# Performance work log

Hardware: AMD Instinct MI355X
Metric: run time of the kernel (lower is better)

Reference implementation:

```python
import jax, jax.numpy as jnp
import numpy as np

B, G, S, GS, P = 32, 512, 128, 32, 10
C, H, RED = 384, 6, 16
HID = 4 * C
D = C // H
SCALE = D ** -0.5

def _gelu(x):
    return jax.nn.gelu(x, approximate=False)

def _ln(x, g, b):
    m = jnp.mean(x, -1, keepdims=True)
    v = jnp.var(x, -1, keepdims=True)
    return (x - m) * jax.lax.rsqrt(v + 1e-5) * g + b

def _split_qkv(x, W):
    Bn, T, Cc = x.shape
    qkv = (x @ W).reshape(Bn, T, 3, H, D).transpose(2, 0, 3, 1, 4)
    return qkv[0], qkv[1], qkv[2]

def _merge(x):
    Bn, Hh, T, Dd = x.shape
    return x.transpose(0, 2, 1, 3).reshape(Bn, T, Hh * Dd)

def _mha(q, k, v):
    a = jax.nn.softmax(jnp.einsum('bhnd,bhmd->bhnm', q, k) * SCALE, axis=-1)
    return jnp.einsum('bhnm,bhmd->bhnd', a, v)

def _forward(x, center1, center2, neighborhood, prompt_embeddings, ln1_g, ln1_b, Wqkv, Wproj, bproj, gate, ln2_g, ln2_b, W1, b1, W2, b2, ad_down_W, ad_down_b, ad_up_W, ad_up_b, ad_gate, bn_g, bn_b, bn_mean, bn_var, ln3_g, ln3_b, a1_Wqkv, a1_Wproj, a1_bproj, ad1_down_W, ad1_down_b, ad1_up_W, ad1_up_b, idx, center_idx, group_size, if_maxmean, pro_cof, center_cof):
    Bx, Ntok, Cc = x.shape
    # prompt dropout is identity in eval
    prompt = jnp.broadcast_to(prompt_embeddings, (Bx, P, Cc))
    # --- gated dual self / prompt-cross attention ---
    xn = _ln(x, ln1_g, ln1_b)
    q, k, v = _split_qkv(xn, Wqkv)
    xs = _mha(q, k, v)                                  # [B,H,N,D]
    _, pk, pv = _split_qkv(prompt, Wqkv)
    pa = jax.nn.softmax(jnp.einsum('bhnd,bhpd->bhnp', q, pk) * SCALE, axis=-1)
    px = jnp.einsum('bhnp,bhpd->bhnd', gate * pa, pv)   # learned gate per head
    x = x + (_merge(xs) + _merge(px)) @ Wproj + bproj
    # --- MLP + gated bottleneck adapter residual ---
    h = _gelu(_ln(x, ln2_g, ln2_b) @ W1 + b1) @ W2 + b2
    h_ad = h + _gelu(h @ ad_down_W + ad_down_b) @ ad_up_W + ad_up_b
    x = ad_gate * h_ad + x
    cls_x = x[:, :1]
    xt = x[:, 1:]                                       # [B,G,C]
    flat = xt.reshape(Bx * G, Cc)
    x_nb = flat[idx].reshape(Bx * S, group_size, Cc)    # KNN neighborhoods
    x_ct = flat[center_idx].reshape(Bx, S, Cc)          # center features
    # NOTE: original normalizes `neighborhood` by its std, but result is unused
    # --- local self-attention (attn1 over norm3) on each neighborhood ---
    nq, nk, nv = _split_qkv(_ln(x_nb, ln3_g, ln3_b), a1_Wqkv)
    no = _mha(nq, nk, nv)
    x_nb = x_nb + _merge(no) @ a1_Wproj + a1_bproj
    knn = x_nb.reshape(Bx, S, group_size, Cc)
    lc = jnp.max(knn, axis=2)
    if if_maxmean:
        lc = lc + jnp.mean(knn, axis=2)
    # BatchNorm1d (eval, running stats) + GELU over channel dim
    lc = _gelu((lc - bn_mean) * jax.lax.rsqrt(bn_var + 1e-5) * bn_g + bn_b)
    vis = lc + center_cof * x_ct                        # [B,S,C]
    # --- propagate: de_neighbors == S so sorted-topk == full weighted sum ---
    d = jnp.sum((center1[:, :, None, :] - center2[:, None, :, :]) ** 2, axis=-1)  # [B,G,S]
    w = 1.0 / (d + 1e-8)
    w = w / jnp.sum(w, axis=-1, keepdims=True)
    interp = jnp.einsum('bns,bsc->bnc', w, vis)
    xt = xt + pro_cof * interp
    out = jnp.concatenate([cls_x, xt], axis=1)
    # adapter1
    out = out + _gelu(out @ ad1_down_W + ad1_down_b) @ ad1_up_W + ad1_up_b
    return out

def setup_inputs():
    ks = jax.random.split(jax.random.key(0), 20)
    r = lambda i, shape, s=0.02: jax.random.normal(ks[i], shape, jnp.float32) * s
    return {
        'x': jax.random.normal(ks[0], (B, G + 1, C), jnp.float32),
        'center1': jax.random.normal(ks[1], (B, G, 3), jnp.float32),
        'center2': jax.random.normal(ks[2], (B, S, 3), jnp.float32),
        'neighborhood': jax.random.normal(ks[3], (B, S, GS, 3), jnp.float32),
        'prompt_embeddings': r(4, (P, C)),
        'ln1_g': jnp.ones(C), 'ln1_b': jnp.zeros(C),
        'Wqkv': r(5, (C, 3 * C)),
        'Wproj': r(6, (C, C)), 'bproj': jnp.zeros(C),
        'gate': jax.random.normal(ks[7], (1, H, 1, 1), jnp.float32),
        'ln2_g': jnp.ones(C), 'ln2_b': jnp.zeros(C),
        'W1': r(8, (C, HID)), 'b1': jnp.zeros(HID),
        'W2': r(9, (HID, C)), 'b2': jnp.zeros(C),
        'ad_down_W': r(10, (C, RED)), 'ad_down_b': jnp.zeros(RED),
        'ad_up_W': r(11, (RED, C)), 'ad_up_b': jnp.zeros(C),
        'ad_gate': jax.random.normal(ks[12], (), jnp.float32),
        'bn_g': jnp.ones(C), 'bn_b': jnp.zeros(C),
        'bn_mean': jnp.zeros(C), 'bn_var': jnp.ones(C),
        'ln3_g': jnp.ones(C), 'ln3_b': jnp.zeros(C),
        'a1_Wqkv': r(13, (C, 3 * C)),
        'a1_Wproj': r(14, (C, C)), 'a1_bproj': jnp.zeros(C),
        'ad1_down_W': r(15, (C, RED)), 'ad1_down_b': jnp.zeros(RED),
        'ad1_up_W': r(16, (RED, C)), 'ad1_up_b': jnp.zeros(C),
        'idx': jax.random.randint(ks[17], (B * S * GS,), 0, B * G),
        'center_idx': jax.random.randint(ks[18], (B * S,), 0, B * G),
        'group_size': GS,
        'if_maxmean': 1,
        'pro_cof': 1,
        'center_cof': 1,
    }

def reference(x, center1, center2, neighborhood, prompt_embeddings, ln1_g, ln1_b, Wqkv, Wproj, bproj, gate, ln2_g, ln2_b, W1, b1, W2, b2, ad_down_W, ad_down_b, ad_up_W, ad_up_b, ad_gate, bn_g, bn_b, bn_mean, bn_var, ln3_g, ln3_b, a1_Wqkv, a1_Wproj, a1_bproj, ad1_down_W, ad1_down_b, ad1_up_W, ad1_up_b, idx, center_idx, group_size, if_maxmean, pro_cof, center_cof):
    return _forward(x, center1, center2, neighborhood, prompt_embeddings, ln1_g, ln1_b, Wqkv, Wproj, bproj, gate, ln2_g, ln2_b, W1, b1, W2, b2, ad_down_W, ad_down_b, ad_up_W, ad_up_b, ad_gate, bn_g, bn_b, bn_mean, bn_var, ln3_g, ln3_b, a1_Wqkv, a1_Wproj, a1_bproj, ad1_down_W, ad1_down_b, ad1_up_W, ad1_up_b, idx, center_idx, group_size, if_maxmean, pro_cof, center_cof)
```

## Files before the change

kernel.cpp:

```cpp
#include <hip/hip_runtime.h>
#include <hip/hip_bf16.h>
#include <cstdint>
#include <cstddef>

typedef __hip_bfloat16 bf16;
constexpr int TOK = 32 * 513;

typedef __attribute__((ext_vector_type(8))) short short8;
typedef __attribute__((ext_vector_type(4))) float f32x4;

__device__ __forceinline__ float bflo(unsigned u){ return __uint_as_float(u << 16); }
__device__ __forceinline__ float bfhi(unsigned u){ return __uint_as_float(u & 0xffff0000u); }
__device__ __forceinline__ float b2f(bf16 x){ return __bfloat162float(x); }
__device__ __forceinline__ bf16  f2b(float x){ return __float2bfloat16(x); }
__device__ __forceinline__ float geluf(float x){ return 0.5f*x*(1.0f + erff(x*0.70710678118654752f)); }
__device__ __forceinline__ float scal(const int* p){
  const int i = *p;
  if (i > -1000000 && i < 1000000) return (float)i;
  return __int_as_float(i);
}
__device__ __forceinline__ f32x4 mfma16(short8 a, short8 b, f32x4 c){
  return __builtin_amdgcn_mfma_f32_16x16x32_bf16(a, b, c, 0, 0, 0);
}
__device__ __forceinline__ int swzl(int l){ return l ^ ((l >> 3) & 7); }
__device__ __forceinline__ void gload_lds16(const bf16* g, bf16* l){
  __builtin_amdgcn_global_load_lds(
      (const __attribute__((address_space(1))) void*)g,
      (__attribute__((address_space(3))) void*)l, 16, 0, 0);
}

__global__ __launch_bounds__(256) void detect_kernel(const unsigned* __restrict__ x,
                                                     int* __restrict__ flag)
{
  const int t = threadIdx.x;
  bool bad = false;
  for (int i = t; i < 2048; i += 256){
    const unsigned u = x[i];
    const float a = fabsf(bflo(u)), b = fabsf(bfhi(u));
    if (!(a < 1e6f) || !(b < 1e6f)) bad = true;
  }
  __shared__ int s;
  if (t == 0) s = 0;
  __syncthreads();
  const unsigned long long m = __ballot(bad);
  if (m != 0ull && (t & 63) == 0) atomicOr(&s, 1);
  __syncthreads();
  if (t == 0) *flag = s;
}

struct ConvArgs {
  const void* src[34];
  bf16*       dst[34];
  int         n[34];
};
__global__ __launch_bounds__(256) void convert_many(const int* __restrict__ flag, ConvArgs a)
{
  const int ii = blockIdx.y;
  const bool isf = (*flag != 0);
  const int n = a.n[ii];
  const int n8 = n >> 3;
  bf16* d = a.dst[ii];
  if (isf){
    const float4* s = (const float4*)a.src[ii];
    for (int i = blockIdx.x*256 + threadIdx.x; i < n8; i += gridDim.x*256){
      const float4 f0 = s[i*2];
      const float4 f1 = s[i*2 + 1];
      bf16 tmp[8] = {f2b(f0.x),f2b(f0.y),f2b(f0.z),f2b(f0.w),
                     f2b(f1.x),f2b(f1.y),f2b(f1.z),f2b(f1.w)};
      *(uint4*)(d + (size_t)i*8) = *(const uint4*)tmp;
    }
  } else {
    const uint4* s = (const uint4*)a.src[ii];
    for (int i = blockIdx.x*256 + threadIdx.x; i < n8; i += gridDim.x*256){
      ((uint4*)d)[i] = s[i];
    }
  }
  if (blockIdx.x == 0){
    for (int i = n8*8 + threadIdx.x; i < n; i += 256){
      d[i] = isf ? f2b(((const float*)a.src[ii])[i]) : ((const bf16*)a.src[ii])[i];
    }
  }
}

struct ShufArgs {
  const bf16* W[6];
  bf16*       out[6];
  int         N[6];
  int         KT[6];
  int         NT[6];
};
__global__ __launch_bounds__(256) void shuffle_many(ShufArgs a)
{
  const int ii = blockIdx.y;
  const int id = blockIdx.x*256 + threadIdx.x;
  const int KT = a.KT[ii], NT = a.NT[ii], N = a.N[ii];
  if (id >= NT*KT*64) return;
  const int l  = id & 63;
  const int k0 = (id >> 6) % KT;
  const int n0 = (id >> 6) / KT;
  const bf16* W = a.W[ii];
  bf16 tmp[8];
  #pragma unroll
  for (int j = 0; j < 8; j++)
    tmp[j] = W[(size_t)(k0*32 + (l>>4)*8 + j)*N + n0*16 + (l&15)];
  *(uint4*)(a.out[ii] + (size_t)id*8) = *(const uint4*)tmp;
}

template<bool SRC_BF16>
__global__ __launch_bounds__(256) void ln_kernel(const void* __restrict__ src,
    const bf16* __restrict__ g, const bf16* __restrict__ b,
    bf16* __restrict__ out, int rows)
{
  const int wave = (blockIdx.x * blockDim.x + threadIdx.x) >> 6;
  const int lane = threadIdx.x & 63;
  if (wave >= rows) return;
  float v[6]; float s = 0.f, s2 = 0.f;
  #pragma unroll
  for (int i = 0; i < 6; i++){
    const int c = lane + 64*i;
    float x;
    if (SRC_BF16) x = b2f(((const bf16*)src)[(size_t)wave*384 + c]);
    else          x = ((const float*)src)[(size_t)wave*384 + c];
    v[i] = x; s += x; s2 += x*x;
  }
  #pragma unroll
  for (int mm = 32; mm; mm >>= 1){ s += __shfl_xor(s, mm); s2 += __shfl_xor(s2, mm); }
  const float mean = s * (1.f/384.f);
  const float rs = rsqrtf(s2 * (1.f/384.f) - mean*mean + 1e-5f);
  #pragma unroll
  for (int i = 0; i < 6; i++){
    const int c = lane + 64*i;
    out[(size_t)wave*384 + c] = f2b((v[i]-mean)*rs*b2f(g[c]) + b2f(b[c]));
  }
}

template<int EPI>
__global__ __launch_bounds__(256) void mfma_gemm(
    const bf16* __restrict__ A, const bf16* __restrict__ Bsh,
    const bf16* __restrict__ bias, const bf16* __restrict__ resid,
    void* __restrict__ outv, int M, int N, int K)
{
  __shared__ __align__(16) bf16 sA[8*64*8];
  const int t = threadIdx.x, lane = t & 63, w = t >> 6;
  const int l15 = lane & 15, quad = lane >> 4;
  const int wm = w & 1, wn = w >> 1;
  const int m0 = blockIdx.y * 128;
  const int n0t = blockIdx.x * 8 + wn * 4;
  const int KT = K >> 5;
  f32x4 acc[4][4];
  #pragma unroll
  for (int i = 0; i < 4; i++){
    #pragma unroll
    for (int j = 0; j < 4; j++) acc[i][j] = f32x4{0.f,0.f,0.f,0.f};
  }
  const int mtA = 2*w, mtB = 2*w + 1;
  const bf16* gA = A + (size_t)(m0 + mtA*16 + l15)*K + quad*8;
  const bf16* gB = A + (size_t)(m0 + mtB*16 + l15)*K + quad*8;
  bf16* lA = sA + mtA*512;
  bf16* lB = sA + mtB*512;

  for (int ks = 0; ks < KT; ks++){
    gload_lds16(gA + ks*32, lA);
    gload_lds16(gB + ks*32, lB);
    __syncthreads();
    short8 afr[4];
    #pragma unroll
    for (int i = 0; i < 4; i++)
      afr[i] = *(const short8*)(sA + (((wm*4+i)*64 + lane) << 3));
    #pragma unroll
    for (int j = 0; j < 4; j++){
      const short8 b = *(const short8*)(Bsh + ((size_t)((n0t+j)*KT + ks)*64 + lane)*8);
      #pragma unroll
      for (int i = 0; i < 4; i++) acc[i][j] = mfma16(afr[i], b, acc[i][j]);
    }
    __syncthreads();
  }
  #pragma unroll
  for (int i = 0; i < 4; i++){
    #pragma unroll
    for (int r = 0; r < 4; r++){
      const int gm = m0 + (wm*4+i)*16 + quad*4 + r;
      if (gm < M){
        #pragma unroll
        for (int j = 0; j < 4; j++){
          const int gn = (n0t+j)*16 + l15;
          float v = acc[i][j][r];
          const size_t o = (size_t)gm*N + gn;
          if (EPI == 0){ v += b2f(bias[gn]); ((bf16*)outv)[o] = f2b(v); }
          else if (EPI == 1){ ((bf16*)outv)[o] = f2b(v); }
          else if (EPI == 2){ v += b2f(bias[gn]); ((bf16*)outv)[o] = f2b(geluf(v)); }
          else { v += b2f(bias[gn]) + b2f(resid[o]); ((float*)outv)[o] = v; }
        }
      }
    }
  }
}

__global__ __launch_bounds__(256) void pqkv_kernel(const bf16* __restrict__ pe,
    const bf16* __restrict__ Wqkv, float* __restrict__ pq)
{
  const int n  = blockIdx.x*64 + (threadIdx.x & 63);
  const int rg = threadIdx.x >> 6;
  for (int r = rg; r < 10; r += 4){
    float s0 = 0.f, s1 = 0.f;
    for (int c = 0; c < 384; c += 2){
      s0 = fmaf(b2f(pe[(size_t)r*384+c]),   b2f(Wqkv[(size_t)c*1152 + n]),     s0);
      s1 = fmaf(b2f(pe[(size_t)r*384+c+1]), b2f(Wqkv[(size_t)(c+1)*1152 + n]), s1);
    }
    pq[(size_t)r*1152 + n] = s0 + s1;
  }
}

__global__ __launch_bounds__(256) void attn_kernel(
    const bf16* __restrict__ qkv, const float* __restrict__ pq,
    const bf16* __restrict__ gate, bf16* __restrict__ ao)
{
  __shared__ __align__(16) bf16 s_kf[2][8*64*8];
  __shared__ __align__(16) bf16 s_vT[64*72];
  __shared__ __align__(16) bf16 s_p[4*16*64];
  __shared__ __align__(16) bf16 s_pk[16*72];
  __shared__ __align__(16) bf16 s_pvT[64*40];
  const int bh = blockIdx.y;
  const int b = bh / 6, h = bh % 6;
  const int q0 = blockIdx.x * 64;
  const int t = threadIdx.x, lane = t & 63, w = t >> 6;
  const int l15 = lane & 15, quad = lane >> 4;

  const int qtok = q0 + w*16 + l15;
  const int qtokc = qtok < 513 ? qtok : 512;
  const bf16* qp = qkv + (size_t)(b*513 + qtokc)*1152 + h*64 + quad*8;
  const short8 qf0 = *(const short8*)qp;
  const short8 qf1 = *(const short8*)(qp + 32);

  auto issueK = [&](int kb, int buf){
    const int key = kb + w*16 + l15;
    const int keyc = key < 513 ? key : 512;
    const bf16* src = qkv + (size_t)(b*513 + keyc)*1152 + 384 + h*64 + quad*8;
    gload_lds16(src,      &s_kf[buf][((w*2 + 0)*64)*8]);
    gload_lds16(src + 32, &s_kf[buf][((w*2 + 1)*64)*8]);
  };

  const int kp = t & 31, dg = t >> 5;

  {
    const int j = t >> 4, dc = (t & 15) * 4;
    float f[4] = {0.f,0.f,0.f,0.f};
    if (j < 10){
      const float* pk = pq + (size_t)j*1152 + 384 + h*64 + dc;
      f[0]=pk[0]; f[1]=pk[1]; f[2]=pk[2]; f[3]=pk[3];
    }
    bf16 tmp[4] = {f2b(f[0]),f2b(f[1]),f2b(f[2]),f2b(f[3])};
    *(uint2*)(s_pk + j*72 + dc) = *(const uint2*)tmp;
  }
  {
    const int d = t & 63, kg = t >> 6;
    #pragma unroll
    for (int kk = 0; kk < 8; kk++){
      const int key = kg*8 + kk;
      bf16 v = f2b(0.f);
      if (key < 10) v = f2b(pq[(size_t)key*1152 + 768 + h*64 + d]);
      s_pvT[d*40 + key] = v;
    }
  }

  uint4 pv0 = {0,0,0,0}, pv1 = {0,0,0,0};
  {
    const int key0 = 2*kp;
    if (key0 < 513)
      pv0 = *(const uint4*)(qkv + (size_t)(b*513 + key0)*1152 + 768 + h*64 + dg*8);
    if (key0 + 1 < 513)
      pv1 = *(const uint4*)(qkv + (size_t)(b*513 + key0 + 1)*1152 + 768 + h*64 + dg*8);
  }
  issueK(0, 0);
  int cur = 0;

  float m_i[4], l_i[4];
  f32x4 oacc[4];
  #pragma unroll
  for (int r = 0; r < 4; r++){ m_i[r] = -30000.f; l_i[r] = 0.f; }
  #pragma unroll
  for (int nt = 0; nt < 4; nt++) oacc[nt] = f32x4{0.f,0.f,0.f,0.f};
  bf16* myp = s_p + w*16*64;

  for (int kt = 0; kt < 9; kt++){
    const int kb = kt*64;
    __syncthreads();
    {
      const unsigned short* a0 = (const unsigned short*)&pv0;
      const unsigned short* a1 = (const unsigned short*)&pv1;
      unsigned* vt = (unsigned*)s_vT;
      #pragma unroll
      for (int j = 0; j < 8; j++)
        vt[(dg*8 + j)*36 + kp] = (unsigned)a0[j] | ((unsigned)a1[j] << 16);
    }
    __syncthreads();

    f32x4 sreg[4];
    #pragma unroll
    for (int nt = 0; nt < 4; nt++){
      const short8 kf0 = *(const short8*)(&s_kf[cur][((nt*2 + 0)*64 + lane)*8]);
      const short8 kf1 = *(const short8*)(&s_kf[cur][((nt*2 + 1)*64 + lane)*8]);
      f32x4 acc = mfma16(qf0, kf0, f32x4{0.f,0.f,0.f,0.f});
      acc = mfma16(qf1, kf1, acc);
      const bool kvalid = (kb + nt*16 + l15) < 513;
      #pragma unroll
      for (int r = 0; r < 4; r++)
        sreg[nt][r] = kvalid ? acc[r]*0.125f : -30000.f;
    }

    if (kt < 8){
      issueK(kb + 64, cur ^ 1);
      const int key0 = kb + 64 + 2*kp;
      pv0 = {0,0,0,0}; pv1 = {0,0,0,0};
      if (key0 < 513)
        pv0 = *(const uint4*)(qkv + (size_t)(b*513 + key0)*1152 + 768 + h*64 + dg*8);
      if (key0 + 1 < 513)
        pv1 = *(const uint4*)(qkv + (size_t)(b*513 + key0 + 1)*1152 + 768 + h*64 + dg*8);
    }

    float alpha[4];
    #pragma unroll
    for (int r = 0; r < 4; r++){
      float mx = fmaxf(fmaxf(sreg[0][r], sreg[1][r]), fmaxf(sreg[2][r], sreg[3][r]));
      #pragma unroll
      for (int mm = 8; mm; mm >>= 1) mx = fmaxf(mx, __shfl_xor(mx, mm));
      const float mn = fmaxf(m_i[r], mx);
      alpha[r] = __expf(m_i[r] - mn);
      m_i[r] = mn;
      float ps = 0.f;
      #pragma unroll
      for (int nt = 0; nt < 4; nt++){
        const float p = __expf(sreg[nt][r] - mn);
        sreg[nt][r] = p; ps += p;
      }
      #pragma unroll
      for (int mm = 8; mm; mm >>= 1) ps += __shfl_xor(ps, mm);
      l_i[r] = l_i[r]*alpha[r] + ps;
    }
    #pragma unroll
    for (int nt = 0; nt < 4; nt++){
      #pragma unroll
      for (int r = 0; r < 4; r++)
        myp[(quad*4 + r)*64 + nt*16 + l15] = f2b(sreg[nt][r]);
    }
    #pragma unroll
    for (int nt = 0; nt < 4; nt++){
      #pragma unroll
      for (int r = 0; r < 4; r++) oacc[nt][r] *= alpha[r];
    }
    const short8* ap = (const short8*)(myp + l15*64);
    #pragma unroll
    for (int nt = 0; nt < 4; nt++){
      const short8* bv = (const short8*)(s_vT + (nt*16 + l15)*72);
      oacc[nt] = mfma16(ap[quad],     bv[quad],     oacc[nt]);
      oacc[nt] = mfma16(ap[4 + quad], bv[4 + quad], oacc[nt]);
    }
    cur ^= 1;
  }

  f32x4 sp;
  {
    f32x4 acc = f32x4{0.f,0.f,0.f,0.f};
    const short8* bp = (const short8*)(s_pk + l15*72);
    acc = mfma16(qf0, bp[quad],     acc);
    acc = mfma16(qf1, bp[4 + quad], acc);
    #pragma unroll
    for (int r = 0; r < 4; r++)
      sp[r] = (l15 < 10) ? acc[r]*0.125f : -30000.f;
  }
  float psr[4];
  #pragma unroll
  for (int r = 0; r < 4; r++){
    float mx = sp[r];
    #pragma unroll
    for (int mm = 8; mm; mm >>= 1) mx = fmaxf(mx, __shfl_xor(mx, mm));
    const float p = __expf(sp[r] - mx);
    float ps = p;
    #pragma unroll
    for (int mm = 8; mm; mm >>= 1) ps += __shfl_xor(ps, mm);
    psr[r] = ps;
    myp[(quad*4 + r)*64 + l15]      = f2b(p);
    myp[(quad*4 + r)*64 + 16 + l15] = f2b(0.f);
  }
  f32x4 pva[4];
  {
    const short8* ap = (const short8*)(myp + l15*64);
    #pragma unroll
    for (int nt = 0; nt < 4; nt++){
      const short8* bv = (const short8*)(s_pvT + (nt*16 + l15)*40);
      pva[nt] = mfma16(ap[quad], bv[quad], f32x4{0.f,0.f,0.f,0.f});
    }
  }

  const float gh = b2f(gate[h]);
  #pragma unroll
  for (int r = 0; r < 4; r++){
    const int tok = q0 + w*16 + quad*4 + r;
    if (tok < 513){
      const float invl = 1.f/l_i[r];
      const float gps  = gh/psr[r];
      #pragma unroll
      for (int nt = 0; nt < 4; nt++){
        const float val = oacc[nt][r]*invl + pva[nt][r]*gps;
        ao[(size_t)(b*513 + tok)*384 + h*64 + nt*16 + l15] = f2b(val);
      }
    }
  }
}

template<bool MID>
__global__ __launch_bounds__(256) void adapter_kernel(
    const void* __restrict__ src,
    const bf16* __restrict__ Wd, const bf16* __restrict__ bd,
    const bf16* __restrict__ Wu, const bf16* __restrict__ bu,
    const bf16* __restrict__ p_gate,
    const bf16* __restrict__ g3, const bf16* __restrict__ b3,
    const int* __restrict__ flag,
    float* __restrict__ xres, bf16* __restrict__ xln3,
    void* __restrict__ out)
{
  __shared__ float s_h[4][384];
  const int wv = threadIdx.x >> 6, lane = threadIdx.x & 63;
  const int row = blockIdx.x*4 + wv;
  float v[6];
  #pragma unroll
  for (int i = 0; i < 6; i++){
    const int c = lane + 64*i;
    float x;
    if (MID) x = b2f(((const bf16*)src)[(size_t)row*384 + c]);
    else     x = ((const float*)src)[(size_t)row*384 + c];
    v[i] = x; s_h[wv][c] = x;
  }
  const int o = lane & 15, p = lane >> 4;
  float part = 0.f;
  #pragma unroll 4
  for (int j = 0; j < 96; j++)
    part = fmaf(s_h[wv][p*96 + j], b2f(Wd[(size_t)(p*96 + j)*16 + o]), part);
  part += __shfl_xor(part, 16);
  part += __shfl_xor(part, 32);
  const float y = geluf(part + b2f(bd[o]));
  float up[6] = {0.f,0.f,0.f,0.f,0.f,0.f};
  #pragma unroll
  for (int o2 = 0; o2 < 16; o2++){
    const float yo = __shfl(y, o2);
    #pragma unroll
    for (int i = 0; i < 6; i++)
      up[i] = fmaf(yo, b2f(Wu[(size_t)o2*384 + lane + 64*i]), up[i]);
  }
  if (MID){
    const float g = b2f(p_gate[0]);
    float nv[6]; float s = 0.f, s2 = 0.f;
    #pragma unroll
    for (int i = 0; i < 6; i++){
      const int c = lane + 64*i;
      const float had = v[i] + up[i] + b2f(bu[c]);
      const float nx = g*had + xres[(size_t)row*384 + c];
      xres[(size_t)row*384 + c] = nx;
      nv[i] = nx; s += nx; s2 += nx*nx;
    }
    const int boff = row % 513;
    if (boff != 0){
      #pragma unroll
      for (int mm = 32; mm; mm >>= 1){ s += __shfl_xor(s, mm); s2 += __shfl_xor(s2, mm); }
      const float mean = s * (1.f/384.f);
      const float rs = rsqrtf(s2 * (1.f/384.f) - mean*mean + 1e-5f);
      const int r3 = (row/513)*512 + boff - 1;
      #pragma unroll
      for (int i = 0; i < 6; i++){
        const int c = lane + 64*i;
        xln3[(size_t)r3*384 + c] = f2b((nv[i]-mean)*rs*b2f(g3[c]) + b2f(b3[c]));
      }
    }
  } else {
    const bool isf = (*flag != 0);
    #pragma unroll
    for (int i = 0; i < 6; i++){
      const int c = lane + 64*i;
      const float ov = v[i] + up[i] + b2f(bu[c]);
      if (isf) ((float*)out)[(size_t)row*384 + c] = ov;
      else     ((bf16*)out)[(size_t)row*384 + c] = f2b(ov);
    }
  }
}

__global__ __launch_bounds__(512, 2) void local_kernel(
    const bf16* __restrict__ qkv3, const float* __restrict__ xres,
    const int* __restrict__ idx, const int* __restrict__ cidx,
    const bf16* __restrict__ Bp, const bf16* __restrict__ bp1,
    const bf16* __restrict__ bng, const bf16* __restrict__ bnb,
    const bf16* __restrict__ bnm, const bf16* __restrict__ bnv,
    const int* __restrict__ p_ifmm, const int* __restrict__ p_ccof,
    float* __restrict__ vis)
{
  __shared__ __align__(16) bf16 sV[3*4*64*8];
  __shared__ __align__(16) bf16 sP[3*2*64*8];
  __shared__ __align__(16) bf16 sO[3*4*64*8];
  __shared__ int s_flat[32];
  __shared__ int s_tok[32];

  const int g = blockIdx.x;
  const int t = threadIdx.x, lane = t & 63, w = t >> 6;
  const int l15 = lane & 15, quad = lane >> 4;
  const int lanez = swzl(lane);

  if (t < 32){
    const int r = idx[g*32 + t];
    s_flat[t] = r;
    s_tok[t]  = (r >> 9)*513 + 1 + (r & 511);
  }
  __syncthreads();

  const int vrowA = t & 31,          vccA = t >> 5;
  const int vrowB = (512 + t) & 31,  vccB = (512 + t) >> 5;
  const int vhA = vccA >> 3, vd0A = (vccA & 7) * 8;
  const int vhB = vccB >> 3, vd0B = (vccB & 7) * 8;
  const bool hasB = (t < 256);

  uint4 svA, svB;
  {
    svA = *(const uint4*)(qkv3 + (size_t)s_flat[vrowA]*1152 + 768 + (0*3 + vhA)*64 + vd0A);
    if (hasB) svB = *(const uint4*)(qkv3 + (size_t)s_flat[vrowB]*1152 + 768 + (0*3 + vhB)*64 + vd0B);
  }

  f32x4 accp[3][2];
  #pragma unroll
  for (int a = 0; a < 3; a++){
    #pragma unroll
    for (int m = 0; m < 2; m++) accp[a][m] = f32x4{0.f,0.f,0.f,0.f};
  }

  #pragma unroll
  for (int hc = 0; hc < 2; hc++){
    {
      const bf16* sa = (const bf16*)&svA;
      #pragma unroll
      for (int j2 = 0; j2 < 8; j2++){
        const int d = vd0A + j2;
        const int L = (vrowA>>3)*16 + (d&15);
        sV[((vhA*4 + (d>>4))*64 + swzl(L))*8 + (vrowA&7)] = sa[j2];
      }
      if (hasB){
        const bf16* sb = (const bf16*)&svB;
        #pragma unroll
        for (int j2 = 0; j2 < 8; j2++){
          const int d = vd0B + j2;
          const int L = (vrowB>>3)*16 + (d&15);
          sV[((vhB*4 + (d>>4))*64 + swzl(L))*8 + (vrowB&7)] = sb[j2];
        }
      }
    }
    __syncthreads();

    if (w < 6){
      const int h = w >> 1, mt = w & 1;
      const size_t qrow = (size_t)s_flat[mt*16 + l15]*1152;
      const int dcol = (hc*3 + h)*64 + quad*8;
      const short8 q0 = *(const short8*)(qkv3 + qrow + dcol);
      const short8 q1 = *(const short8*)(qkv3 + qrow + dcol + 32);
      f32x4 sr[2];
      #pragma unroll
      for (int nt = 0; nt < 2; nt++){
        const size_t krow = (size_t)s_flat[nt*16 + l15]*1152 + 384;
        const short8 k0 = *(const short8*)(qkv3 + krow + dcol);
        const short8 k1 = *(const short8*)(qkv3 + krow + dcol + 32);
        f32x4 acc = mfma16(q0, k0, f32x4{0.f,0.f,0.f,0.f});
        acc = mfma16(q1, k1, acc);
        #pragma unroll
        for (int r = 0; r < 4; r++) sr[nt][r] = acc[r]*0.125f;
      }
      #pragma unroll
      for (int r = 0; r < 4; r++){
        float mx = fmaxf(sr[0][r], sr[1][r]);
        #pragma unroll
        for (int mm = 8; mm; mm >>= 1) mx = fmaxf(mx, __shfl_xor(mx, mm));
        const float e0 = __expf(sr[0][r] - mx), e1 = __expf(sr[1][r] - mx);
        float sm = e0 + e1;
        #pragma unroll
        for (int mm = 8; mm; mm >>= 1) sm += __shfl_xor(sm, mm);
        const float inv = 1.f/sm;
        const int m = quad*4 + r;
        const int L0 = (l15 >> 3)*16       + m;
        const int L1 = (2 + (l15 >> 3))*16 + m;
        sP[((h*2 + mt)*64 + swzl(L0))*8 + (l15 & 7)] = f2b(e0*inv);
        sP[((h*2 + mt)*64 + swzl(L1))*8 + (l15 & 7)] = f2b(e1*inv);
      }
    }
    __syncthreads();

    {
      const int mt = w & 1, nt = w >> 1;
      const int k0w = nt >> 1, qdw = (nt & 1)*2 + (l15 >> 3), jw = l15 & 7;
      #pragma unroll
      for (int h = 0; h < 3; h++){
        const short8 a = *(const short8*)(sP + ((h*2 + mt)*64 + lanez)*8);
        const short8 b = *(const short8*)(sV + ((h*4 + nt)*64 + lanez)*8);
        const f32x4 o = mfma16(a, b, f32x4{0.f,0.f,0.f,0.f});
        #pragma unroll
        for (int r = 0; r < 4; r++){
          const int L = qdw*16 + quad*4 + r;
          sO[((h*4 + mt*2 + k0w)*64 + swzl(L))*8 + jw] = f2b(o[r]);
        }
      }
    }
    __syncthreads();

    if (hc == 0){
      svA = *(const uint4*)(qkv3 + (size_t)s_flat[vrowA]*1152 + 768 + (3 + vhA)*64 + vd0A);
      if (hasB) svB = *(const uint4*)(qkv3 + (size_t)s_flat[vrowB]*1152 + 768 + (3 + vhB)*64 + vd0B);
    }

    #pragma unroll
    for (int h = 0; h < 3; h++){
      short8 afr[2][2];
      #pragma unroll
      for (int mt = 0; mt < 2; mt++){
        #pragma unroll
        for (int k0l = 0; k0l < 2; k0l++)
          afr[mt][k0l] = *(const short8*)(sO + ((h*4 + mt*2 + k0l)*64 + lanez)*8);
      }
      const int hg2 = (hc*3 + h)*2;
      #pragma unroll
      for (int tt = 0; tt < 3; tt++){
        const int nt = w*3 + tt;
        #pragma unroll
        for (int k0l = 0; k0l < 2; k0l++){
          const short8 b = *(const short8*)(Bp + ((size_t)(nt*12 + hg2 + k0l)*64 + lane)*8);
          accp[tt][0] = mfma16(afr[0][k0l], b, accp[tt][0]);
          accp[tt][1] = mfma16(afr[1][k0l], b, accp[tt][1]);
        }
      }
    }
    __syncthreads();
  }

  const float fmm  = scal(p_ifmm);
  const float ccof = scal(p_ccof);
  const int cr = cidx[g];
  const int ctok = (cr >> 9)*513 + 1 + (cr & 511);
  #pragma unroll
  for (int tt = 0; tt < 3; tt++){
    const int n = (w*3 + tt)*16 + l15;
    const float bb = b2f(bp1[n]);
    float mx = -3e30f, sm = 0.f;
    #pragma unroll
    for (int mt = 0; mt < 2; mt++){
      #pragma unroll
      for (int r = 0; r < 4; r++){
        const int tok = mt*16 + quad*4 + r;
        const float v = accp[tt][mt][r] + bb + xres[(size_t)s_tok[tok]*384 + n];
        mx = fmaxf(mx, v); sm += v;
      }
    }
    mx = fmaxf(mx, __shfl_xor(mx, 16)); sm += __shfl_xor(sm, 16);
    mx = fmaxf(mx, __shfl_xor(mx, 32)); sm += __shfl_xor(sm, 32);
    if (quad == 0){
      const float lc = (fmm != 0.f) ? (mx + sm*(1.f/32.f)) : mx;
      const float nr = (lc - b2f(bnm[n])) * rsqrtf(b2f(bnv[n]) + 1e-5f) * b2f(bng[n]) + b2f(bnb[n]);
      vis[(size_t)g*384 + n] = geluf(nr) + ccof * xres[(size_t)ctok*384 + n];
    }
  }
}

__global__ __launch_bounds__(256) void interp_kernel(const bf16* __restrict__ c1,
    const bf16* __restrict__ c2, const float* __restrict__ vis,
    const int* __restrict__ p_pcof, float* __restrict__ xres)
{
  __shared__ float s_w[4][128];
  __shared__ float s_red[2];
  const int b = blockIdx.y;
  const int n0 = blockIdx.x * 4;
  const int t = threadIdx.x;
  for (int ni = 0; ni < 4; ni++){
    const int n = n0 + ni;
    float wv = 0.f;
    if (t < 128){
      float d2 = 0.f;
      #pragma unroll
      for (int k = 0; k < 3; k++){
        const float a = b2f(c1[((size_t)b*512 + n)*3 + k]);
        const float c = b2f(c2[((size_t)b*128 + t)*3 + k]);
        const float df = a - c; d2 += df*df;
      }
      wv = 1.f/(d2 + 1e-8f);
    }
    float rsum = wv;
    #pragma unroll
    for (int mm = 32; mm; mm >>= 1) rsum += __shfl_xor(rsum, mm);
    if (((t & 63) == 0) && t < 128) s_red[t >> 6] = rsum;
    __syncthreads();
    const float tot = s_red[0] + s_red[1];
    if (t < 128) s_w[ni][t] = wv / tot;
    __syncthreads();
  }
  float acc1[4], acc2[4];
  #pragma unroll
  for (int ni = 0; ni < 4; ni++){ acc1[ni] = 0.f; acc2[ni] = 0.f; }
  for (int s = 0; s < 128; s++){
    const float* vp = vis + ((size_t)b*128 + s)*384;
    const float v1 = vp[t];
    const float v2 = (t < 128) ? vp[t + 256] : 0.f;
    #pragma unroll
    for (int ni = 0; ni < 4; ni++){
      const float wn = s_w[ni][s];
      acc1[ni] = fmaf(wn, v1, acc1[ni]);
      acc2[ni] = fmaf(wn, v2, acc2[ni]);
    }
  }
  const float pc = scal(p_pcof);
  #pragma unroll
  for (int ni = 0; ni < 4; ni++){
    const int tok = b*513 + 1 + n0 + ni;
    xres[(size_t)tok*384 + t] += pc*acc1[ni];
    if (t < 128) xres[(size_t)tok*384 + t + 256] += pc*acc2[ni];
  }
}

extern "C" void kernel_launch(void* const* d_in, const int* in_sizes, int n_in,
                              void* d_out, int out_size, void* d_ws, size_t ws_size,
                              hipStream_t stream)
{
  (void)n_in; (void)out_size; (void)ws_size;
  const int*  idx   = (const int*)d_in[35];
  const int*  cidx  = (const int*)d_in[36];
  const int*  ifmm  = (const int*)d_in[38];
  const int*  pcof  = (const int*)d_in[39];
  const int*  ccof  = (const int*)d_in[40];

  size_t off = 0;
  auto alloc = [&](size_t bytes) -> void* {
    void* p = (char*)d_ws + off; off += (bytes + 255) & ~(size_t)255; return p;
  };
  int*   flag = (int*)  alloc(sizeof(int));
  float* xres = (float*)alloc((size_t)TOK*384*4);
  bf16*  slab = (bf16*) alloc((size_t)TOK*1536*2);
  bf16*  xn   = (bf16*) alloc((size_t)TOK*384*2);
  float* pq   = (float*)alloc((size_t)10*1152*4);
  bf16*  Bq   = (bf16*) alloc((size_t)72*12*64*8*2);
  bf16*  Bp   = (bf16*) alloc((size_t)24*12*64*8*2);
  bf16*  Bqkv = (bf16*) alloc((size_t)72*12*64*8*2);
  bf16*  Bw1  = (bf16*) alloc((size_t)96*12*64*8*2);
  bf16*  Bw2  = (bf16*) alloc((size_t)24*48*64*8*2);
  bf16*  Bwp  = (bf16*) alloc((size_t)24*12*64*8*2);

  bf16*  qkvb = slab;
  bf16*  x_c  = slab + (size_t)TOK*1152;
  bf16*  h1   = slab;
  bf16*  qkv3 = slab;
  bf16*  xln3 = slab + (size_t)TOK*1152;
  bf16*  ao   = xn;
  bf16*  hbuf = xn;
  float* visb = (float*)xn;

  const int conv_ids[34] = {0,1,2,4,5,6,7,8,9,10,11,12,13,14,15,16,17,
                            18,19,20,21,22,23,24,25,26,27,28,29,30,31,32,33,34};
  ConvArgs ca;
  bf16* canon[41];
  int maxn = 1;
  for (int k = 0; k < 34; k++){
    const int i = conv_ids[k];
    const int n = in_sizes[i];
    bf16* dst = (i == 0) ? x_c : (bf16*)alloc((size_t)n*2);
    ca.src[k] = d_in[i]; ca.dst[k] = dst; ca.n[k] = n;
    canon[i] = dst;
    if (n > maxn) maxn = n;
  }
  detect_kernel<<<dim3(1), dim3(256), 0, stream>>>((const unsigned*)d_in[0], flag);
  {
    int gx = (maxn/8 + 255) / 256; if (gx > 512) gx = 512; if (gx < 1) gx = 1;
    convert_many<<<dim3(gx, 34), dim3(256), 0, stream>>>(flag, ca);
  }

  const bf16 *x_in = canon[0], *c1 = canon[1], *c2 = canon[2], *pe = canon[4],
             *ln1g = canon[5], *ln1b = canon[6], *Wqkv = canon[7], *Wproj = canon[8],
             *bproj = canon[9], *gate = canon[10], *ln2g = canon[11], *ln2b = canon[12],
             *W1 = canon[13], *b1 = canon[14], *W2 = canon[15], *b2v = canon[16],
             *adW = canon[17], *adb = canon[18], *adU = canon[19], *adub = canon[20],
             *adg = canon[21], *bng = canon[22], *bnb = canon[23], *bnm = canon[24],
             *bnv = canon[25], *ln3g = canon[26], *ln3b = canon[27], *a1W = canon[28],
             *a1P = canon[29], *a1pb = canon[30], *d1W = canon[31], *d1b = canon[32],
             *u1W = canon[33], *u1b = canon[34];

  {
    ShufArgs sa;
    sa.W[0]=a1W;   sa.out[0]=Bq;   sa.N[0]=1152; sa.KT[0]=12; sa.NT[0]=72;
    sa.W[1]=a1P;   sa.out[1]=Bp;   sa.N[1]=384;  sa.KT[1]=12; sa.NT[1]=24;
    sa.W[2]=Wqkv;  sa.out[2]=Bqkv; sa.N[2]=1152; sa.KT[2]=12; sa.NT[2]=72;
    sa.W[3]=W1;    sa.out[3]=Bw1;  sa.N[3]=1536; sa.KT[3]=12; sa.NT[3]=96;
    sa.W[4]=W2;    sa.out[4]=Bw2;  sa.N[4]=384;  sa.KT[4]=48; sa.NT[4]=24;
    sa.W[5]=Wproj; sa.out[5]=Bwp;  sa.N[5]=384;  sa.KT[5]=12; sa.NT[5]=24;
    shuffle_many<<<dim3(288, 6), dim3(256), 0, stream>>>(sa);
  }

  ln_kernel<true><<<dim3((TOK*64)/256), dim3(256), 0, stream>>>((const void*)x_in, ln1g, ln1b, xn, TOK);
  mfma_gemm<1><<<dim3(9,129), dim3(256), 0, stream>>>(xn, Bqkv, nullptr, nullptr, qkvb, TOK, 1152, 384);
  pqkv_kernel<<<dim3(18), dim3(256), 0, stream>>>(pe, Wqkv, pq);
  attn_kernel<<<dim3(9,192), dim3(256), 0, stream>>>(qkvb, pq, gate, ao);
  mfma_gemm<3><<<dim3(3,129), dim3(256), 0, stream>>>(ao, Bwp, bproj, x_in, xres, TOK, 384, 384);
  ln_kernel<false><<<dim3((TOK*64)/256), dim3(256), 0, stream>>>((const void*)xres, ln2g, ln2b, xn, TOK);
  mfma_gemm<2><<<dim3(12,129), dim3(256), 0, stream>>>(xn, Bw1, b1, nullptr, h1, TOK, 1536, 384);
  mfma_gemm<0><<<dim3(3,129), dim3(256), 0, stream>>>(h1, Bw2, b2v, nullptr, hbuf, TOK, 384, 1536);
  adapter_kernel<true><<<dim3(TOK/4), dim3(256), 0, stream>>>(
      (const void*)hbuf, adW, adb, adU, adub, adg, ln3g, ln3b, nullptr, xres, xln3, nullptr);
  mfma_gemm<1><<<dim3(9,128), dim3(256), 0, stream>>>(xln3, Bq, nullptr, nullptr, qkv3, 16384, 1152, 384);
  local_kernel<<<dim3(4096), dim3(512), 0, stream>>>(qkv3, xres, idx, cidx, Bp, a1pb,
                                                     bng, bnb, bnm, bnv, ifmm, ccof, visb);
  interp_kernel<<<dim3(128,32), dim3(256), 0, stream>>>(c1, c2, visb, pcof, xres);
  adapter_kernel<false><<<dim3(TOK/4), dim3(256), 0, stream>>>(
      (const void*)xres, d1W, d1b, u1W, u1b, nullptr, nullptr, nullptr, flag, nullptr, nullptr, d_out);
}
```

Measured before the change: 782.7 us.

## Split inverse-distance interpolation into weight precompute and wider apply kernel

Moves the inverse-distance weight computation into its own kernel, one wavefront per (batch, point), which writes normalized weights to a workspace buffer. The apply kernel then handles 16 output points per block with 384 threads, one thread per channel, so each vis value loaded is reused across 16 points instead of 4 and the in-block syncthreads reductions go away. The cost is an extra launch and an 8 MB weight buffer that is written and read back through global memory, with weights fetched by uniform global loads instead of from shared memory.

```diff
diff --git a/kernel.cpp b/kernel.cpp
--- a/kernel.cpp
+++ b/kernel.cpp
@@ -661,57 +661,57 @@
   }
 }
 
-__global__ __launch_bounds__(256) void interp_kernel(const bf16* __restrict__ c1,
-    const bf16* __restrict__ c2, const float* __restrict__ vis,
+__global__ __launch_bounds__(256) void interp_w_kernel(
+    const bf16* __restrict__ c1, const bf16* __restrict__ c2,
+    float* __restrict__ wbuf)
+{
+  const int wv = threadIdx.x >> 6, lane = threadIdx.x & 63;
+  const int pair = blockIdx.x*4 + wv;
+  const int b = pair >> 9, n = pair & 511;
+  const float a0 = b2f(c1[((size_t)b*512 + n)*3 + 0]);
+  const float a1 = b2f(c1[((size_t)b*512 + n)*3 + 1]);
+  const float a2 = b2f(c1[((size_t)b*512 + n)*3 + 2]);
+  float wv2[2];
+  #pragma unroll
+  for (int j = 0; j < 2; j++){
+    const int s = lane + j*64;
+    const float d0 = a0 - b2f(c2[((size_t)b*128 + s)*3 + 0]);
+    const float d1 = a1 - b2f(c2[((size_t)b*128 + s)*3 + 1]);
+    const float d2 = a2 - b2f(c2[((size_t)b*128 + s)*3 + 2]);
+    wv2[j] = 1.f/(d0*d0 + d1*d1 + d2*d2 + 1e-8f);
+  }
+  float sum = wv2[0] + wv2[1];
+  #pragma unroll
+  for (int mm = 32; mm; mm >>= 1) sum += __shfl_xor(sum, mm);
+  const float inv = 1.f/sum;
+  float* wp = wbuf + ((size_t)b*512 + n)*128;
+  wp[lane]      = wv2[0]*inv;
+  wp[lane + 64] = wv2[1]*inv;
+}
+
+__global__ __launch_bounds__(384) void interp_apply_kernel(
+    const float* __restrict__ wbuf, const float* __restrict__ vis,
     const int* __restrict__ p_pcof, float* __restrict__ xres)
 {
-  __shared__ float s_w[4][128];
-  __shared__ float s_red[2];
   const int b = blockIdx.y;
-  const int n0 = blockIdx.x * 4;
+  const int n0 = blockIdx.x * 16;
   const int t = threadIdx.x;
-  for (int ni = 0; ni < 4; ni++){
-    const int n = n0 + ni;
-    float wv = 0.f;
-    if (t < 128){
-      float d2 = 0.f;
-      #pragma unroll
-      for (int k = 0; k < 3; k++){
-        const float a = b2f(c1[((size_t)b*512 + n)*3 + k]);
-        const float c = b2f(c2[((size_t)b*128 + t)*3 + k]);
-        const float df = a - c; d2 += df*df;
-      }
-      wv = 1.f/(d2 + 1e-8f);
-    }
-    float rsum = wv;
-    #pragma unroll
-    for (int mm = 32; mm; mm >>= 1) rsum += __shfl_xor(rsum, mm);
-    if (((t & 63) == 0) && t < 128) s_red[t >> 6] = rsum;
-    __syncthreads();
-    const float tot = s_red[0] + s_red[1];
-    if (t < 128) s_w[ni][t] = wv / tot;
-    __syncthreads();
-  }
-  float acc1[4], acc2[4];
-  #pragma unroll
-  for (int ni = 0; ni < 4; ni++){ acc1[ni] = 0.f; acc2[ni] = 0.f; }
+  float acc[16];
+  #pragma unroll
+  for (int i = 0; i < 16; i++) acc[i] = 0.f;
+  const float* vp = vis + (size_t)b*128*384;
+  const float* wp = wbuf + ((size_t)b*512 + n0)*128;
   for (int s = 0; s < 128; s++){
-    const float* vp = vis + ((size_t)b*128 + s)*384;
-    const float v1 = vp[t];
-    const float v2 = (t < 128) ? vp[t + 256] : 0.f;
-    #pragma unroll
-    for (int ni = 0; ni < 4; ni++){
-      const float wn = s_w[ni][s];
-      acc1[ni] = fmaf(wn, v1, acc1[ni]);
-      acc2[ni] = fmaf(wn, v2, acc2[ni]);
-    }
+    const float v = vp[(size_t)s*384 + t];
+    #pragma unroll
+    for (int i = 0; i < 16; i++)
+      acc[i] = fmaf(wp[(size_t)i*128 + s], v, acc[i]);
   }
   const float pc = scal(p_pcof);
   #pragma unroll
-  for (int ni = 0; ni < 4; ni++){
-    const int tok = b*513 + 1 + n0 + ni;
-    xres[(size_t)tok*384 + t] += pc*acc1[ni];
-    if (t < 128) xres[(size_t)tok*384 + t + 256] += pc*acc2[ni];
+  for (int i = 0; i < 16; i++){
+    const size_t o = (size_t)(b*513 + 1 + n0 + i)*384 + t;
+    xres[o] += pc*acc[i];
   }
 }
 
@@ -735,6 +735,7 @@
   bf16*  slab = (bf16*) alloc((size_t)TOK*1536*2);
   bf16*  xn   = (bf16*) alloc((size_t)TOK*384*2);
   float* pq   = (float*)alloc((size_t)10*1152*4);
+  float* wbuf = (float*)alloc((size_t)32*512*128*4);
   bf16*  Bq   = (bf16*) alloc((size_t)72*12*64*8*2);
   bf16*  Bp   = (bf16*) alloc((size_t)24*12*64*8*2);
   bf16*  Bqkv = (bf16*) alloc((size_t)72*12*64*8*2);
@@ -802,9 +803,10 @@
   adapter_kernel<true><<<dim3(TOK/4), dim3(256), 0, stream>>>(
       (const void*)hbuf, adW, adb, adU, adub, adg, ln3g, ln3b, nullptr, xres, xln3, nullptr);
   mfma_gemm<1><<<dim3(9,128), dim3(256), 0, stream>>>(xln3, Bq, nullptr, nullptr, qkv3, 16384, 1152, 384);
+  interp_w_kernel<<<dim3(4096), dim3(256), 0, stream>>>(c1, c2, wbuf);
   local_kernel<<<dim3(4096), dim3(512), 0, stream>>>(qkv3, xres, idx, cidx, Bp, a1pb,
                                                      bng, bnb, bnm, bnv, ifmm, ccof, visb);
-  interp_kernel<<<dim3(128,32), dim3(256), 0, stream>>>(c1, c2, visb, pcof, xres);
+  interp_apply_kernel<<<dim3(32,32), dim3(384), 0, stream>>>(wbuf, visb, pcof, xres);
   adapter_kernel<false><<<dim3(TOK/4), dim3(256), 0, stream>>>(
       (const void*)xres, d1W, d1b, u1W, u1b, nullptr, nullptr, nullptr, flag, nullptr, nullptr, d_out);
 }
```

Result: slower. 802.4 us (+2.5%).
